# Performance work log

Measured on AMD Instinct MI355X. Metric: run time of the kernel, lower is better.

## Reference

```python
import jax, jax.numpy as jnp
import numpy as np

EPS = 1e-5  # torch LayerNorm default


def setup_inputs() -> dict:
    key = jax.random.key(0)
    ks = jax.random.split(key, 7)
    B, s, i, c, h = 1, 1024, 512, 8, 8
    scale = 0.1
    return {
        "m": jax.random.normal(ks[0], (B, s, i, c), dtype=jnp.float32),
        "ln_gamma": jnp.ones((c,), dtype=jnp.float32),
        "ln_beta": jnp.zeros((c,), dtype=jnp.float32),
        "Wq": jax.random.normal(ks[1], (c * h, c), dtype=jnp.float32) * scale,
        "Wk": jax.random.normal(ks[2], (c, c), dtype=jnp.float32) * scale,
        "Wv": jax.random.normal(ks[3], (c, c), dtype=jnp.float32) * scale,
        "Wg": jax.random.normal(ks[4], (c * h, c), dtype=jnp.float32) * scale,
        "Wo": jax.random.normal(ks[5], (c, c * h), dtype=jnp.float32) * scale,
        "bo": jnp.zeros((c,), dtype=jnp.float32),
    }


def reference(m, ln_gamma, ln_beta, Wq, Wk, Wv, Wg, Wo, bo):
    c = Wk.shape[0]
    h = Wq.shape[0] // c
    B, s, i, _ = m.shape

    # LayerNorm over the channel dim c
    mu = jnp.mean(m, axis=-1, keepdims=True)
    var = jnp.mean(jnp.square(m - mu), axis=-1, keepdims=True)
    x = (m - mu) * jax.lax.rsqrt(var + EPS) * ln_gamma + ln_beta  # (B,s,i,c)

    # projections (torch Linear: y = x @ W.T)
    q = (x @ Wq.T).reshape(B, s, i, h, c).mean(axis=1)            # (B,i,h,c) mean-pooled query
    k = x @ Wk.T                                                   # (B,s,i,c)
    v = x @ Wv.T                                                   # (B,s,i,c)
    gate = jax.nn.sigmoid(x @ Wg.T).reshape(B, s, i, h, c)        # (B,s,i,h,c)

    # attention logits over the column axis t (=s), softmax along t (dim=-3 of b t i h)
    a = jnp.einsum('bihc,btic->btih', q, k) * (c ** -0.5)          # (B,s,i,h)
    a = jax.nn.softmax(a, axis=1)

    o = gate * jnp.einsum('btih,btic->btihc', a, v)               # (B,s,i,h,c)
    o = o.reshape(B, s, i, h * c)
    return o @ Wo.T + bo                                           # (B,s,i,c)
```

## Files before the change

### kernel.cpp

```cpp
#include <hip/hip_runtime.h>

namespace {
constexpr int S = 1024, I = 512, C = 8, H = 8;
constexpr int R = 4;
constexpr float LNEPS = 1e-5f;
constexpr float SCALE = 0.35355339059327373f;
}

__device__ __forceinline__ float dot8(const float x[8], float4 a, float4 b) {
    float r = x[0] * a.x;
    r += x[1] * a.y; r += x[2] * a.z; r += x[3] * a.w;
    r += x[4] * b.x; r += x[5] * b.y; r += x[6] * b.z; r += x[7] * b.w;
    return r;
}

__device__ __forceinline__ void ln8(float4 a, float4 b, const float gm[8],
                                    const float bt[8], float x[8]) {
    x[0] = a.x; x[1] = a.y; x[2] = a.z; x[3] = a.w;
    x[4] = b.x; x[5] = b.y; x[6] = b.z; x[7] = b.w;
    float mu = 0.f;
#pragma unroll
    for (int c = 0; c < 8; c++) mu += x[c];
    mu *= 0.125f;
    float var = 0.f;
#pragma unroll
    for (int c = 0; c < 8; c++) { float d = x[c] - mu; var += d * d; }
    var *= 0.125f;
    float inv = rsqrtf(var + LNEPS);
#pragma unroll
    for (int c = 0; c < 8; c++) x[c] = (x[c] - mu) * inv * gm[c] + bt[c];
}

__global__ __launch_bounds__(256, 3) void fused(
    const float* __restrict__ m, const float* __restrict__ gamma,
    const float* __restrict__ beta, const float* __restrict__ Wq,
    const float* __restrict__ Wk, const float* __restrict__ Wv,
    const float* __restrict__ Wg, const float* __restrict__ Wo,
    const float* __restrict__ bo, float* __restrict__ out) {
    __shared__ __align__(16) float sWoT[512];
    __shared__ __align__(16) float swred[4 * 8];
    __shared__ __align__(16) float sxbar[8];
    __shared__ __align__(16) float sqk[64];
    __shared__ __align__(16) float srden[8];

    int t = threadIdx.x;
    int w = t >> 6;
    int i = blockIdx.x;

#pragma unroll
    for (int k = 0; k < 2; k++) {
        int idx = t + 256 * k;
        int j = idx & 63, c2 = idx >> 6;
        sWoT[j * 8 + c2] = Wo[c2 * 64 + j];
    }

    float gm[8], bt[8];
#pragma unroll
    for (int c = 0; c < 8; c++) { gm[c] = gamma[c]; bt[c] = beta[c]; }

    const float4* m4 = (const float4*)m;
    float x[R][8];
    float acc[8];
#pragma unroll
    for (int c = 0; c < 8; c++) acc[c] = 0.f;
#pragma unroll
    for (int r = 0; r < R; r++) {
        int row = (t + 256 * r) * I + i;
        ln8(m4[row * 2], m4[row * 2 + 1], gm, bt, x[r]);
#pragma unroll
        for (int c = 0; c < 8; c++) acc[c] += x[r][c];
    }
#pragma unroll
    for (int d = 1; d < 64; d <<= 1)
#pragma unroll
        for (int c = 0; c < 8; c++) acc[c] += __shfl_xor(acc[c], d, 64);
    if ((t & 63) == 0) {
#pragma unroll
        for (int c = 0; c < 8; c++) swred[w * 8 + c] = acc[c];
    }
    __syncthreads();
    if (t < 8)
        sxbar[t] = swred[t] + swred[8 + t] + swred[16 + t] + swred[24 + t];
    __syncthreads();
    if (t < 64) {
        int h = t >> 3, c2 = t & 7;
        float a = 0.f;
#pragma unroll
        for (int c = 0; c < 8; c++) {
            float qc = 0.f;
#pragma unroll
            for (int c3 = 0; c3 < 8; c3++)
                qc += sxbar[c3] * Wq[(h * 8 + c) * 8 + c3];
            a += qc * Wk[c * 8 + c2];
        }
        sqk[t] = a * (SCALE / 1024.0f);
    }
    __syncthreads();

    const float4* sqk4 = (const float4*)sqk;
    float p[R][8];
    {
        float e[8];
#pragma unroll
        for (int h = 0; h < 8; h++) {
            float4 q0 = sqk4[h * 2], q1 = sqk4[h * 2 + 1];
            float s = 0.f;
#pragma unroll
            for (int r = 0; r < R; r++) {
                p[r][h] = __expf(dot8(x[r], q0, q1));
                s += p[r][h];
            }
            e[h] = s;
        }
#pragma unroll
        for (int d = 1; d < 64; d <<= 1)
#pragma unroll
            for (int h = 0; h < 8; h++) e[h] += __shfl_xor(e[h], d, 64);
        if ((t & 63) == 0) {
#pragma unroll
            for (int h = 0; h < 8; h++) swred[w * 8 + h] = e[h];
        }
    }
    __syncthreads();
    if (t < 8)
        srden[t] =
            1.0f / (swred[t] + swred[8 + t] + swred[16 + t] + swred[24 + t]);
    __syncthreads();

#pragma unroll
    for (int h = 0; h < 8; h++) {
        float rd = srden[h];
#pragma unroll
        for (int r = 0; r < R; r++) p[r][h] *= rd;
    }

    const float4* Wv4 = (const float4*)Wv;
    const float4* Wg4 = (const float4*)Wg;
    const float4* sWoT4 = (const float4*)sWoT;

    float oacc[R][8];
#pragma unroll
    for (int r = 0; r < R; r++)
#pragma unroll
        for (int c2 = 0; c2 < 8; c2++) oacc[r][c2] = bo[c2];

#pragma unroll 1
    for (int c = 0; c < 8; c++) {
        float4 wv0 = Wv4[c * 2], wv1 = Wv4[c * 2 + 1];
        float vr[R];
#pragma unroll
        for (int r = 0; r < R; r++) vr[r] = dot8(x[r], wv0, wv1);
#pragma unroll 2
        for (int h = 0; h < 8; h++) {
            int hc = h * 8 + c;
            float4 wg0 = Wg4[hc * 2], wg1 = Wg4[hc * 2 + 1];
            float4 wo0 = sWoT4[hc * 2], wo1 = sWoT4[hc * 2 + 1];
            float o_[R];
#pragma unroll
            for (int r = 0; r < R; r++) {
                float z = dot8(x[r], wg0, wg1);
                float gate = __builtin_amdgcn_rcpf(1.0f + __expf(-z));
                o_[r] = gate * p[r][h] * vr[r];
            }
#pragma unroll
            for (int r = 0; r < R; r++) {
                oacc[r][0] += o_[r] * wo0.x; oacc[r][1] += o_[r] * wo0.y;
                oacc[r][2] += o_[r] * wo0.z; oacc[r][3] += o_[r] * wo0.w;
                oacc[r][4] += o_[r] * wo1.x; oacc[r][5] += o_[r] * wo1.y;
                oacc[r][6] += o_[r] * wo1.z; oacc[r][7] += o_[r] * wo1.w;
            }
        }
    }
    float4* out4 = (float4*)out;
#pragma unroll
    for (int r = 0; r < R; r++) {
        int row = (t + 256 * r) * I + i;
        out4[row * 2] = make_float4(oacc[r][0], oacc[r][1], oacc[r][2], oacc[r][3]);
        out4[row * 2 + 1] = make_float4(oacc[r][4], oacc[r][5], oacc[r][6], oacc[r][7]);
    }
}

extern "C" void kernel_launch(void* const* d_in, const int* in_sizes, int n_in,
                              void* d_out, int out_size, void* d_ws, size_t ws_size,
                              hipStream_t stream) {
    const float* m     = (const float*)d_in[0];
    const float* gamma = (const float*)d_in[1];
    const float* beta  = (const float*)d_in[2];
    const float* Wq    = (const float*)d_in[3];
    const float* Wk    = (const float*)d_in[4];
    const float* Wv    = (const float*)d_in[5];
    const float* Wg    = (const float*)d_in[6];
    const float* Wo    = (const float*)d_in[7];
    const float* bo    = (const float*)d_in[8];
    float* out = (float*)d_out;

    fused<<<I, 256, 0, stream>>>(m, gamma, beta, Wq, Wk, Wv, Wg, Wo, bo, out);
}
```

Before: 123.7 us.

## Use 1024-thread blocks with one row per thread and packed f32x2 math

Each block now launches 1024 threads, so each thread handles a single s-row instead of four, and the block reductions sum over 16 waves. Dot products and the Wo accumulation use two-wide float vectors, which the compiler can map to packed FMA instructions, and the inner loops are fully unrolled. The goal is more parallel threads per column to hide memory latency, plus fewer instructions in the gate/output loop. In exchange, each thread now reloads the Wg and Wv weights and recomputes its own share of the weight-dependent work, with no reuse across rows.

```diff
diff --git a/kernel.cpp b/kernel.cpp
--- a/kernel.cpp
+++ b/kernel.cpp
@@ -1,17 +1,23 @@
 #include <hip/hip_runtime.h>
 
 namespace {
-constexpr int S = 1024, I = 512, C = 8, H = 8;
-constexpr int R = 4;
+constexpr int S = 1024, I = 512;
 constexpr float LNEPS = 1e-5f;
 constexpr float SCALE = 0.35355339059327373f;
 }
 
-__device__ __forceinline__ float dot8(const float x[8], float4 a, float4 b) {
-    float r = x[0] * a.x;
-    r += x[1] * a.y; r += x[2] * a.z; r += x[3] * a.w;
-    r += x[4] * b.x; r += x[5] * b.y; r += x[6] * b.z; r += x[7] * b.w;
-    return r;
+typedef float f32x2 __attribute__((ext_vector_type(2)));
+
+__device__ __forceinline__ float dot8p(const f32x2 x2[4], float4 a, float4 b) {
+    f32x2 w0; w0.x = a.x; w0.y = a.y;
+    f32x2 w1; w1.x = a.z; w1.y = a.w;
+    f32x2 w2; w2.x = b.x; w2.y = b.y;
+    f32x2 w3; w3.x = b.z; w3.y = b.w;
+    f32x2 acc = x2[0] * w0;
+    acc = x2[1] * w1 + acc;
+    acc = x2[2] * w2 + acc;
+    acc = x2[3] * w3 + acc;
+    return acc.x + acc.y;
 }
 
 __device__ __forceinline__ void ln8(float4 a, float4 b, const float gm[8],
@@ -31,14 +37,14 @@
     for (int c = 0; c < 8; c++) x[c] = (x[c] - mu) * inv * gm[c] + bt[c];
 }
 
-__global__ __launch_bounds__(256, 3) void fused(
+__global__ __launch_bounds__(1024, 2) void fused(
     const float* __restrict__ m, const float* __restrict__ gamma,
     const float* __restrict__ beta, const float* __restrict__ Wq,
     const float* __restrict__ Wk, const float* __restrict__ Wv,
     const float* __restrict__ Wg, const float* __restrict__ Wo,
     const float* __restrict__ bo, float* __restrict__ out) {
     __shared__ __align__(16) float sWoT[512];
-    __shared__ __align__(16) float swred[4 * 8];
+    __shared__ __align__(16) float swred[16 * 8];
     __shared__ __align__(16) float sxbar[8];
     __shared__ __align__(16) float sqk[64];
     __shared__ __align__(16) float srden[8];
@@ -47,10 +53,8 @@
     int w = t >> 6;
     int i = blockIdx.x;
 
-#pragma unroll
-    for (int k = 0; k < 2; k++) {
-        int idx = t + 256 * k;
-        int j = idx & 63, c2 = idx >> 6;
+    if (t < 512) {
+        int j = t & 63, c2 = t >> 6;
         sWoT[j * 8 + c2] = Wo[c2 * 64 + j];
     }
 
@@ -59,28 +63,34 @@
     for (int c = 0; c < 8; c++) { gm[c] = gamma[c]; bt[c] = beta[c]; }
 
     const float4* m4 = (const float4*)m;
-    float x[R][8];
-    float acc[8];
+    int row = t * I + i;
+    float x[8];
+    ln8(m4[row * 2], m4[row * 2 + 1], gm, bt, x);
+
+    f32x2 x2[4];
 #pragma unroll
-    for (int c = 0; c < 8; c++) acc[c] = 0.f;
+    for (int j = 0; j < 4; j++) { x2[j].x = x[2 * j]; x2[j].y = x[2 * j + 1]; }
+
+    {
+        float acc[8];
 #pragma unroll
-    for (int r = 0; r < R; r++) {
-        int row = (t + 256 * r) * I + i;
-        ln8(m4[row * 2], m4[row * 2 + 1], gm, bt, x[r]);
+        for (int c = 0; c < 8; c++) acc[c] = x[c];
 #pragma unroll
-        for (int c = 0; c < 8; c++) acc[c] += x[r][c];
-    }
+        for (int d = 1; d < 64; d <<= 1)
 #pragma unroll
-    for (int d = 1; d < 64; d <<= 1)
+            for (int c = 0; c < 8; c++) acc[c] += __shfl_xor(acc[c], d, 64);
+        if ((t & 63) == 0) {
 #pragma unroll
-        for (int c = 0; c < 8; c++) acc[c] += __shfl_xor(acc[c], d, 64);
-    if ((t & 63) == 0) {
-#pragma unroll
-        for (int c = 0; c < 8; c++) swred[w * 8 + c] = acc[c];
+            for (int c = 0; c < 8; c++) swred[w * 8 + c] = acc[c];
+        }
     }
     __syncthreads();
-    if (t < 8)
-        sxbar[t] = swred[t] + swred[8 + t] + swred[16 + t] + swred[24 + t];
+    if (t < 8) {
+        float s = 0.f;
+#pragma unroll
+        for (int ww = 0; ww < 16; ww++) s += swred[ww * 8 + t];
+        sxbar[t] = s;
+    }
     __syncthreads();
     if (t < 64) {
         int h = t >> 3, c2 = t & 7;
@@ -98,19 +108,13 @@
     __syncthreads();
 
     const float4* sqk4 = (const float4*)sqk;
-    float p[R][8];
+    float p[8];
     {
         float e[8];
 #pragma unroll
         for (int h = 0; h < 8; h++) {
-            float4 q0 = sqk4[h * 2], q1 = sqk4[h * 2 + 1];
-            float s = 0.f;
-#pragma unroll
-            for (int r = 0; r < R; r++) {
-                p[r][h] = __expf(dot8(x[r], q0, q1));
-                s += p[r][h];
-            }
-            e[h] = s;
+            p[h] = __expf(dot8p(x2, sqk4[h * 2], sqk4[h * 2 + 1]));
+            e[h] = p[h];
         }
 #pragma unroll
         for (int d = 1; d < 64; d <<= 1)
@@ -122,62 +126,50 @@
         }
     }
     __syncthreads();
-    if (t < 8)
-        srden[t] =
-            1.0f / (swred[t] + swred[8 + t] + swred[16 + t] + swred[24 + t]);
+    if (t < 8) {
+        float s = 0.f;
+#pragma unroll
+        for (int ww = 0; ww < 16; ww++) s += swred[ww * 8 + t];
+        srden[t] = 1.0f / s;
+    }
     __syncthreads();
 
 #pragma unroll
-    for (int h = 0; h < 8; h++) {
-        float rd = srden[h];
-#pragma unroll
-        for (int r = 0; r < R; r++) p[r][h] *= rd;
-    }
+    for (int h = 0; h < 8; h++) p[h] *= srden[h];
 
     const float4* Wv4 = (const float4*)Wv;
     const float4* Wg4 = (const float4*)Wg;
-    const float4* sWoT4 = (const float4*)sWoT;
+    const f32x2* sWoT2 = (const f32x2*)sWoT;
 
-    float oacc[R][8];
+    float v[8];
 #pragma unroll
-    for (int r = 0; r < R; r++)
+    for (int c = 0; c < 8; c++)
+        v[c] = dot8p(x2, Wv4[c * 2], Wv4[c * 2 + 1]);
+
+    f32x2 oacc2[4];
 #pragma unroll
-        for (int c2 = 0; c2 < 8; c2++) oacc[r][c2] = bo[c2];
+    for (int j = 0; j < 4; j++) {
+        oacc2[j].x = bo[2 * j]; oacc2[j].y = bo[2 * j + 1];
+    }
 
-#pragma unroll 1
+#pragma unroll
     for (int c = 0; c < 8; c++) {
-        float4 wv0 = Wv4[c * 2], wv1 = Wv4[c * 2 + 1];
-        float vr[R];
 #pragma unroll
-        for (int r = 0; r < R; r++) vr[r] = dot8(x[r], wv0, wv1);
-#pragma unroll 2
         for (int h = 0; h < 8; h++) {
             int hc = h * 8 + c;
-            float4 wg0 = Wg4[hc * 2], wg1 = Wg4[hc * 2 + 1];
-            float4 wo0 = sWoT4[hc * 2], wo1 = sWoT4[hc * 2 + 1];
-            float o_[R];
-#pragma unroll
-            for (int r = 0; r < R; r++) {
-                float z = dot8(x[r], wg0, wg1);
-                float gate = __builtin_amdgcn_rcpf(1.0f + __expf(-z));
-                o_[r] = gate * p[r][h] * vr[r];
-            }
-#pragma unroll
-            for (int r = 0; r < R; r++) {
-                oacc[r][0] += o_[r] * wo0.x; oacc[r][1] += o_[r] * wo0.y;
-                oacc[r][2] += o_[r] * wo0.z; oacc[r][3] += o_[r] * wo0.w;
-                oacc[r][4] += o_[r] * wo1.x; oacc[r][5] += o_[r] * wo1.y;
-                oacc[r][6] += o_[r] * wo1.z; oacc[r][7] += o_[r] * wo1.w;
-            }
+            float z = dot8p(x2, Wg4[hc * 2], Wg4[hc * 2 + 1]);
+            float gate = __builtin_amdgcn_rcpf(1.0f + __expf(-z));
+            float o_ = gate * p[h] * v[c];
+            f32x2 o2; o2.x = o_; o2.y = o_;
+            oacc2[0] = o2 * sWoT2[hc * 4 + 0] + oacc2[0];
+            oacc2[1] = o2 * sWoT2[hc * 4 + 1] + oacc2[1];
+            oacc2[2] = o2 * sWoT2[hc * 4 + 2] + oacc2[2];
+            oacc2[3] = o2 * sWoT2[hc * 4 + 3] + oacc2[3];
         }
     }
     float4* out4 = (float4*)out;
-#pragma unroll
-    for (int r = 0; r < R; r++) {
-        int row = (t + 256 * r) * I + i;
-        out4[row * 2] = make_float4(oacc[r][0], oacc[r][1], oacc[r][2], oacc[r][3]);
-        out4[row * 2 + 1] = make_float4(oacc[r][4], oacc[r][5], oacc[r][6], oacc[r][7]);
-    }
+    out4[row * 2] = make_float4(oacc2[0].x, oacc2[0].y, oacc2[1].x, oacc2[1].y);
+    out4[row * 2 + 1] = make_float4(oacc2[2].x, oacc2[2].y, oacc2[3].x, oacc2[3].y);
 }
 
 extern "C" void kernel_launch(void* const* d_in, const int* in_sizes, int n_in,
@@ -194,5 +186,5 @@
     const float* bo    = (const float*)d_in[8];
     float* out = (float*)d_out;
 
-    fused<<<I, 256, 0, stream>>>(m, gamma, beta, Wq, Wk, Wv, Wg, Wo, bo, out);
+    fused<<<I, 1024, 0, stream>>>(m, gamma, beta, Wq, Wk, Wv, Wg, Wo, bo, out);
 }
```

Result: faster. 120.9 us (-2.2%).
